# Kernel optimization log

Measured on AMD Instinct MI355X. Metric: run time of the kernel, lower is better.

Reference implementation:

```python
import jax, jax.numpy as jnp
import numpy as np

GH, GW = 1024, 1024  # image-like grid graph, N = GH*GW nodes


def _grid_edge_index(h, w):
    idx = np.arange(h * w, dtype=np.int32).reshape(h, w)
    r = np.concatenate([idx[:, :-1].ravel(), idx[:, 1:].ravel(), idx[:-1, :].ravel(), idx[1:, :].ravel()])
    c = np.concatenate([idx[:, 1:].ravel(), idx[:, :-1].ravel(), idx[1:, :].ravel(), idx[:-1, :].ravel()])
    return np.stack([r, c]).astype(np.int32)


def setup_inputs():
    key = jax.random.key(0)
    ks = jax.random.split(key, 10)
    n = GH * GW
    ei = jnp.asarray(_grid_edge_index(GH, GW))
    yy, xx = np.meshgrid(np.arange(GH), np.arange(GW), indexing="ij")
    pos = jnp.asarray((np.stack([xx, yy], -1).reshape(n, 2) / float(GH)).astype(np.float32))
    x = jax.random.normal(ks[0], (n, 5), jnp.float32)
    s1, s2, s3, s4 = 5 ** -0.5, 16 ** -0.5, 32 ** -0.5, 8 ** -0.5
    return {
        "x": x, "pos": pos, "edge_index": ei,
        "W1": jax.random.normal(ks[1], (5, 16), jnp.float32) * s1,
        "W1r": jax.random.normal(ks[2], (5, 16), jnp.float32) * s1,
        "b1": jnp.zeros((16,), jnp.float32),
        "W2": jax.random.normal(ks[3], (16, 32), jnp.float32) * s2,
        "W2r": jax.random.normal(ks[4], (16, 32), jnp.float32) * s2,
        "b2": jnp.zeros((32,), jnp.float32),
        "lin1_w": jax.random.normal(ks[5], (32, 8), jnp.float32) * s3,
        "lin1_b": jnp.zeros((8,), jnp.float32),
        "lin2_w": jax.random.normal(ks[6], (8, 2), jnp.float32) * s4,
        "lin2_b": jnp.zeros((2,), jnp.float32),
    }


def _spline_conv_k1(x, row, col, evalid, W, Wr, b, n):
    # SplineConv(dim=1, kernel_size=1): single basis fn == 1, edge_attr cancels.
    # out_i = mean_{(j->i)} x_j @ W + x_i @ Wr + b   (aggr='mean', target = col)
    xw = x @ W
    seg = jnp.where(evalid, col, n)  # invalid edges -> dump segment n
    msg = jnp.where(evalid[:, None], xw[row], 0.0)
    s = jax.ops.segment_sum(msg, seg, num_segments=n + 1)[:n]
    cnt = jax.ops.segment_sum(evalid.astype(x.dtype), seg, num_segments=n + 1)[:n]
    return s / jnp.maximum(cnt, 1.0)[:, None] + x @ Wr + b


def _normalized_cut(row, col, edge_attr, evalid, n):
    seg = jnp.where(evalid, row, n)
    deg = jax.ops.segment_sum(evalid.astype(edge_attr.dtype), seg, num_segments=n + 1)[:n]
    inv = jnp.where(deg > 0, 1.0 / jnp.maximum(deg, 1.0), 0.0)
    return edge_attr * (inv[row] + inv[col])


def _heavy_edge_match(row, col, w, evalid, n):
    # graclus-style heavy-edge matching, deterministic parallel mutual-max variant:
    # each node proposes its max-weight neighbor; mutual proposals merge.
    ar = jnp.arange(n, dtype=jnp.int32)
    seg = jnp.where(evalid, row, n)
    wm = jnp.where(evalid, w, -jnp.inf)
    best = jax.ops.segment_max(wm, seg, num_segments=n + 1)[:n]
    is_best = evalid & (w == best[row])
    partner = jax.ops.segment_min(jnp.where(is_best, col, n), seg, num_segments=n + 1)[:n]
    partner = jnp.where(partner >= n, ar, partner).astype(jnp.int32)
    mutual = partner[partner] == ar
    return jnp.where(mutual, jnp.minimum(ar, partner), ar)


def _forward(x, pos, edge_index, W1, W1r, b1, W2, W2r, b2, lin1_w, lin1_b, lin2_w, lin2_b):
    n = x.shape[0]
    row, col = edge_index[0], edge_index[1]
    ev0 = jnp.ones(row.shape[0], dtype=bool)
    ar = jnp.arange(n, dtype=jnp.int32)

    # GNN1: relu(SplineConv) then LeakyReLU(0.1)
    x1 = jax.nn.leaky_relu(jax.nn.relu(_spline_conv_k1(x, row, col, ev0, W1, W1r, b1, n)), 0.1)

    # normalized_cut_2d on 1-d pseudo-pos x0[:,0]; graclus; max_pool
    attr1 = jnp.abs(x[row, 0] - x[col, 0])
    c1 = _heavy_edge_match(row, col, _normalized_cut(row, col, attr1, ev0, n), ev0, n)
    valid1 = c1 == ar
    xp = jax.ops.segment_max(x1, c1, num_segments=n)  # cluster-wise max pool
    xp = jnp.where(valid1[:, None], xp, 0.0)
    cnt1 = jax.ops.segment_sum(jnp.ones((n,), x.dtype), c1, num_segments=n)
    posp = jax.ops.segment_sum(pos, c1, num_segments=n) / jnp.maximum(cnt1, 1.0)[:, None]
    row2, col2 = c1[row], c1[col]
    ev2 = row2 != col2  # drop intra-cluster (self-loop) edges

    # GNN2 (kernel_size=1 => pooled Cartesian edge_attr unused) + LeakyReLU(0.1)
    x2 = jax.nn.leaky_relu(jax.nn.relu(_spline_conv_k1(xp, row2, col2, ev2, W2, W2r, b2, n)), 0.1)

    # normalized_cut on pooled 2-d pos; graclus; max_pool_x; global_mean_pool
    d = posp[row2] - posp[col2]
    attr2 = jnp.sqrt(jnp.sum(d * d, axis=1) + 1e-12)
    c2 = _heavy_edge_match(row2, col2, _normalized_cut(row2, col2, attr2, ev2, n), ev2, n)
    seg2 = jnp.where(valid1, c2, n)
    x3 = jax.ops.segment_max(x2, seg2, num_segments=n + 1)[:n]
    cnt2 = jax.ops.segment_sum(valid1.astype(x.dtype), seg2, num_segments=n + 1)[:n]
    valid2 = cnt2 > 0
    x3 = jnp.where(valid2[:, None], x3, 0.0)
    pooled = jnp.sum(x3, axis=0) / jnp.sum(valid2.astype(x.dtype))  # single graph -> mean over clusters

    h = jax.nn.leaky_relu(pooled @ lin1_w + lin1_b, 0.1)
    return h @ lin2_w + lin2_b  # == x[0], shape [2]


def reference(x, pos, edge_index, W1, W1r, b1, W2, W2r, b2, lin1_w, lin1_b, lin2_w, lin2_b):
    return _forward(x, pos, edge_index, W1, W1r, b1, W2, W2r, b2, lin1_w, lin1_b, lin2_w, lin2_b)
```

## Files before the change

kernel.cpp:

```cpp
#include <hip/hip_runtime.h>
#include <math.h>

typedef long long i64;
typedef unsigned long long u64;

#define GWD 1024
#define GMSK 1023
#define GSH 10

__device__ __forceinline__ int deg_of(int m) {
  int xx = m & GMSK, yy = m >> GSH;
  return (xx > 0) + (xx < GMSK) + (yy > 0) + (yy < GMSK);
}

__global__ __launch_bounds__(256)
void kA_match1(const float* __restrict__ x, int* __restrict__ partner1, int n) {
#pragma clang fp contract(off)
  int m = blockIdx.x * 256 + threadIdx.x;
  if (m >= n) return;
  int xx = m & GMSK, yy = m >> GSH;
  bool vW = xx > 0, vE = xx < GMSK, vN = yy > 0, vS = yy < GMSK;
  int cnt = (int)vW + (int)vE + (int)vN + (int)vS;
  float invi = 1.0f / (float)cnt;
  float xm0 = x[(i64)m * 5];
  float best = -INFINITY;
  int pr = n;
#define NB1(valid, J)                                                  \
  if (valid) {                                                         \
    int j = (J);                                                       \
    float a0 = x[(i64)j * 5];                                          \
    float w = fabsf(xm0 - a0) * (invi + 1.0f / (float)deg_of(j));      \
    if (w > best) { best = w; pr = j; }                                \
  }
  NB1(vN, m - GWD)
  NB1(vW, m - 1)
  NB1(vE, m + 1)
  NB1(vS, m + GWD)
#undef NB1
  partner1[m] = pr;
}

__device__ __forceinline__ void conv1_static(const float* __restrict__ x, int m,
                                             const float* w1, const float* w1r,
                                             const float* b1, float (&out)[16]) {
  int xx = m & GMSK, yy = m >> GSH;
  bool vW = xx > 0, vE = xx < GMSK, vN = yy > 0, vS = yy < GMSK;
  int cnt = (int)vW + (int)vE + (int)vN + (int)vS;
  float s0 = 0.f, s1 = 0.f, s2 = 0.f, s3 = 0.f, s4 = 0.f;
#define ACC1(valid, J)                                     \
  if (valid) {                                             \
    const float* xj = x + (i64)(J) * 5;                    \
    s0 += xj[0]; s1 += xj[1]; s2 += xj[2];                 \
    s3 += xj[3]; s4 += xj[4];                              \
  }
  ACC1(vN, m - GWD)
  ACC1(vW, m - 1)
  ACC1(vE, m + 1)
  ACC1(vS, m + GWD)
#undef ACC1
  const float* xm = x + (i64)m * 5;
  float m0 = xm[0], m1 = xm[1], m2 = xm[2], m3 = xm[3], m4 = xm[4];
  float cf = (float)cnt;
#pragma unroll
  for (int f = 0; f < 16; ++f) {
    float a  = s0 * w1[f] + s1 * w1[16 + f] + s2 * w1[32 + f] + s3 * w1[48 + f] + s4 * w1[64 + f];
    float rt = m0 * w1r[f] + m1 * w1r[16 + f] + m2 * w1r[32 + f] + m3 * w1r[48 + f] + m4 * w1r[64 + f];
    out[f] = fmaxf(a / cf + rt + b1[f], 0.0f);
  }
}

__global__ __launch_bounds__(256)
void kB_pool1(const float* __restrict__ x, const float* __restrict__ pos,
              const int* __restrict__ partner1,
              const float* __restrict__ W1, const float* __restrict__ W1r,
              const float* __restrict__ b1,
              int* __restrict__ c1, float* __restrict__ xp,
              float* __restrict__ posp, int n) {
  __shared__ float w1s[80], w1rs[80], b1s[16];
  for (int t = threadIdx.x; t < 80; t += 256) { w1s[t] = W1[t]; w1rs[t] = W1r[t]; }
  if (threadIdx.x < 16) b1s[threadIdx.x] = b1[threadIdx.x];
  __syncthreads();
  int m = blockIdx.x * 256 + threadIdx.x;
  if (m >= n) return;
  int p = partner1[m];
  bool mut = (partner1[p] == m);
  int head = mut ? min(m, p) : m;
  c1[m] = head;
  if (head != m) return;

  float px = pos[(i64)m * 2], py = pos[(i64)m * 2 + 1];
  if (mut) {
    px = (px + pos[(i64)p * 2]) * 0.5f;
    py = (py + pos[(i64)p * 2 + 1]) * 0.5f;
  }
  posp[(i64)m * 2] = px;
  posp[(i64)m * 2 + 1] = py;

  float v[16];
  conv1_static(x, m, w1s, w1rs, b1s, v);
  if (mut) {
    float u[16];
    conv1_static(x, p, w1s, w1rs, b1s, u);
#pragma unroll
    for (int f = 0; f < 16; ++f) v[f] = fmaxf(v[f], u[f]);
  }
#pragma unroll
  for (int f = 0; f < 16; ++f) xp[(i64)m * 16 + f] = v[f];
}

__device__ __forceinline__ int dcount(const int* __restrict__ c1, int q, int cq) {
  int xx = q & GMSK, yy = q >> GSH;
  int d = 0;
  if (yy > 0    && c1[q - GWD] != cq) ++d;
  if (xx > 0    && c1[q - 1]   != cq) ++d;
  if (xx < GMSK && c1[q + 1]   != cq) ++d;
  if (yy < GMSK && c1[q + GWD] != cq) ++d;
  return d;
}

__global__ __launch_bounds__(256)
void kC_deg2(const int* __restrict__ partner1, const int* __restrict__ c1,
             int* __restrict__ deg2, int n) {
  int m = blockIdx.x * 256 + threadIdx.x;
  if (m >= n) return;
  if (c1[m] != m) return;
  int p = partner1[m];
  bool mut = (partner1[p] == m);
  int d = dcount(c1, m, m);
  if (mut) d += dcount(c1, p, m);
  deg2[m] = d;
}

__global__ __launch_bounds__(256)
void kD_match2(const int* __restrict__ partner1, const int* __restrict__ c1,
               const float* __restrict__ posp, const int* __restrict__ deg2,
               int* __restrict__ partner2, int n) {
#pragma clang fp contract(off)
  int i = blockIdx.x * 256 + threadIdx.x;
  if (i >= n) return;
  if (c1[i] != i) return;
  int p = partner1[i];
  bool mut = (partner1[p] == i);
  float pix = posp[(i64)i * 2], piy = posp[(i64)i * 2 + 1];
  int di = deg2[i];
  float invi = (di > 0) ? 1.0f / (float)di : 0.0f;
  float best = -INFINITY;
  int bc = n;
#define NB2(valid, J)                                                   \
  if (valid) {                                                          \
    int j = (J);                                                        \
    int cu = c1[j];                                                     \
    if (cu != i) {                                                      \
      float dx = pix - posp[(i64)cu * 2];                               \
      float dy = piy - posp[(i64)cu * 2 + 1];                           \
      float attr = sqrtf((dx * dx + dy * dy) + 1e-12f);                 \
      int dc = deg2[cu];                                                \
      float invc = (dc > 0) ? 1.0f / (float)dc : 0.0f;                  \
      float w = attr * (invi + invc);                                   \
      if (w > best) { best = w; bc = cu; }                              \
      else if (w == best && cu < bc) bc = cu;                           \
    }                                                                   \
  }
  {
    int xx = i & GMSK, yy = i >> GSH;
    NB2(yy > 0, i - GWD)
    NB2(xx > 0, i - 1)
    NB2(xx < GMSK, i + 1)
    NB2(yy < GMSK, i + GWD)
  }
  if (mut) {
    int qx = p & GMSK, qy = p >> GSH;
    NB2(qy > 0, p - GWD)
    NB2(qx > 0, p - 1)
    NB2(qx < GMSK, p + 1)
    NB2(qy < GMSK, p + GWD)
  }
#undef NB2
  partner2[i] = (bc >= n) ? i : bc;
}

__device__ __forceinline__ bool l2head(const int* __restrict__ c1,
                                       const int* __restrict__ partner2, int i, int n) {
  if (i >= n || c1[i] != i) return false;
  int p2 = partner2[i];
  bool mut2 = (p2 != i) && (partner2[p2] == i);
  return !(mut2 && p2 < i);
}

__global__ __launch_bounds__(256)
void kP_count(const int* __restrict__ c1, const int* __restrict__ partner2,
              int* __restrict__ blockCounts, int n) {
  int i = blockIdx.x * 256 + threadIdx.x;
  bool a = l2head(c1, partner2, i, n);
  u64 b = __ballot(a);
  __shared__ int wc4[4];
  int lane = threadIdx.x & 63, wv = threadIdx.x >> 6;
  if (lane == 0) wc4[wv] = __popcll(b);
  __syncthreads();
  if (threadIdx.x == 0) blockCounts[blockIdx.x] = wc4[0] + wc4[1] + wc4[2] + wc4[3];
}

__global__ __launch_bounds__(256)
void kP_scan(const int* __restrict__ blockCounts, int* __restrict__ blockOffsets,
             int* __restrict__ countBuf, int nblk,
             const float* __restrict__ W2, const float* __restrict__ W2r,
             float* __restrict__ W2T, float* __restrict__ W2rT) {
  int t = threadIdx.x;
  for (int e = t; e < 512; e += 256) {
    int k = e >> 5, f = e & 31;
    W2T[f * 16 + k]  = W2[e];
    W2rT[f * 16 + k] = W2r[e];
  }
  __shared__ int tsum[256];
  __shared__ int toff[256];
  int per = (nblk + 255) / 256;
  int base = t * per;
  int s = 0;
  for (int k = 0; k < per; ++k) { int q = base + k; if (q < nblk) s += blockCounts[q]; }
  tsum[t] = s;
  __syncthreads();
  if (t == 0) {
    int a = 0;
    for (int k = 0; k < 256; ++k) { toff[k] = a; a += tsum[k]; }
    *countBuf = a;
  }
  __syncthreads();
  int off = toff[t];
  for (int k = 0; k < per; ++k) {
    int q = base + k;
    if (q < nblk) { blockOffsets[q] = off; off += blockCounts[q]; }
  }
}

__global__ __launch_bounds__(256)
void kP_write(const int* __restrict__ c1, const int* __restrict__ partner2,
              const int* __restrict__ blockOffsets, int* __restrict__ L, int n) {
  int i = blockIdx.x * 256 + threadIdx.x;
  bool a = l2head(c1, partner2, i, n);
  u64 b = __ballot(a);
  int lane = threadIdx.x & 63, wv = threadIdx.x >> 6;
  __shared__ int woff[4];
  if (lane == 0) woff[wv] = __popcll(b);
  __syncthreads();
  int pre = 0;
  for (int k = 0; k < wv; ++k) pre += woff[k];
  int rank = __popcll(b & ((lane == 0) ? 0ull : ((1ull << lane) - 1ull)));
  if (a) L[blockOffsets[blockIdx.x] + pre + rank] = i;
}

#define DECL16(P) \
  float P##0=0.f,P##1=0.f,P##2=0.f,P##3=0.f,P##4=0.f,P##5=0.f,P##6=0.f,P##7=0.f, \
        P##8=0.f,P##9=0.f,P##10=0.f,P##11=0.f,P##12=0.f,P##13=0.f,P##14=0.f,P##15=0.f

#define LOAD16(P, ptr) do { const float* _q=(ptr); \
  P##0=_q[0]; P##1=_q[1]; P##2=_q[2]; P##3=_q[3]; P##4=_q[4]; P##5=_q[5]; P##6=_q[6]; P##7=_q[7]; \
  P##8=_q[8]; P##9=_q[9]; P##10=_q[10]; P##11=_q[11]; P##12=_q[12]; P##13=_q[13]; P##14=_q[14]; P##15=_q[15]; } while(0)

#define ADD16(P, ptr) do { const float* _q=(ptr); \
  P##0+=_q[0]; P##1+=_q[1]; P##2+=_q[2]; P##3+=_q[3]; P##4+=_q[4]; P##5+=_q[5]; P##6+=_q[6]; P##7+=_q[7]; \
  P##8+=_q[8]; P##9+=_q[9]; P##10+=_q[10]; P##11+=_q[11]; P##12+=_q[12]; P##13+=_q[13]; P##14+=_q[14]; P##15+=_q[15]; } while(0)

#define MUL16(P, v) do { float _v=(v); \
  P##0*=_v; P##1*=_v; P##2*=_v; P##3*=_v; P##4*=_v; P##5*=_v; P##6*=_v; P##7*=_v; \
  P##8*=_v; P##9*=_v; P##10*=_v; P##11*=_v; P##12*=_v; P##13*=_v; P##14*=_v; P##15*=_v; } while(0)

#define GATHER_MEMBER(P, CNT, m, cid) do {                                      \
  int _m = (m); int _mx = _m & GMSK, _my = _m >> GSH;                            \
  if (_my > 0)    { int _c = c1[_m - GWD]; if (_c != (cid)) { ++CNT; ADD16(P, xp + (i64)_c * 16); } } \
  if (_mx > 0)    { int _c = c1[_m - 1];   if (_c != (cid)) { ++CNT; ADD16(P, xp + (i64)_c * 16); } } \
  if (_mx < GMSK) { int _c = c1[_m + 1];   if (_c != (cid)) { ++CNT; ADD16(P, xp + (i64)_c * 16); } } \
  if (_my < GMSK) { int _c = c1[_m + GWD]; if (_c != (cid)) { ++CNT; ADD16(P, xp + (i64)_c * 16); } } \
} while(0)

__global__ __launch_bounds__(256)
void kE6_conv2_reduce(const int* __restrict__ partner1, const int* __restrict__ c1,
                      const int* __restrict__ partner2, const float* __restrict__ xp,
                      const float* __restrict__ W2T, const float* __restrict__ W2rT,
                      const float* __restrict__ b2,
                      const int* __restrict__ L, const int* __restrict__ countBuf,
                      float* __restrict__ partials) {
  int count = *countBuf;
  if ((i64)blockIdx.x * 128 >= (i64)count) {
    if (threadIdx.x < 33) partials[(i64)threadIdx.x * gridDim.x + blockIdx.x] = 0.f;
    return;
  }
  int gt = blockIdx.x * 256 + threadIdx.x;
  int pi = gt >> 1;
  int which = gt & 1;
  bool active = pi < count;
  bool doconv = false;
  DECL16(s); DECL16(hh); int cnt = 0;
  if (active) {
    int h = L[pi];
    int p2 = partner2[h];
    bool mut2 = (p2 != h) && (partner2[p2] == h);
    int myhead = which ? p2 : h;
    doconv = (which == 0) || mut2;
    if (doconv) {
      int pm = partner1[myhead];
      bool mm = (partner1[pm] == myhead);
      GATHER_MEMBER(s, cnt, myhead, myhead);
      if (mm) GATHER_MEMBER(s, cnt, pm, myhead);
      LOAD16(hh, xp + (i64)myhead * 16);
    }
  }
  float cf = (float)(cnt > 1 ? cnt : 1);
  float inv = 1.0f / cf;
  MUL16(s, inv);

  __shared__ float sm[4 * 33];
  int lane = threadIdx.x & 63, wv = threadIdx.x >> 6;

  for (int f = 0; f < 32; ++f) {
    const float4* wc = (const float4*)(W2T + (f << 4));
    float4 c0 = wc[0], c1v = wc[1], c2 = wc[2], c3 = wc[3];
    const float4* wr = (const float4*)(W2rT + (f << 4));
    float4 r0 = wr[0], r1 = wr[1], r2 = wr[2], r3 = wr[3];
    float bf = b2[f];
    float val = 0.f;
    if (doconv) {
      float a = s0 * c0.x + s1 * c0.y + s2 * c0.z + s3 * c0.w
              + s4 * c1v.x + s5 * c1v.y + s6 * c1v.z + s7 * c1v.w
              + s8 * c2.x + s9 * c2.y + s10 * c2.z + s11 * c2.w
              + s12 * c3.x + s13 * c3.y + s14 * c3.z + s15 * c3.w
              + hh0 * r0.x + hh1 * r0.y + hh2 * r0.z + hh3 * r0.w
              + hh4 * r1.x + hh5 * r1.y + hh6 * r1.z + hh7 * r1.w
              + hh8 * r2.x + hh9 * r2.y + hh10 * r2.z + hh11 * r2.w
              + hh12 * r3.x + hh13 * r3.y + hh14 * r3.z + hh15 * r3.w
              + bf;
      val = fmaxf(a, 0.0f);
    }
    float pmx = fmaxf(val, __shfl_xor(val, 1, 64));
    float contrib = (which == 0) ? pmx : 0.f;
    for (int o = 32; o >= 2; o >>= 1) contrib += __shfl_down(contrib, o, 64);
    if (lane == 0) sm[wv * 33 + f] = contrib;
  }
  {
    float v = (active && which == 0) ? 1.f : 0.f;
    for (int o = 32; o >= 2; o >>= 1) v += __shfl_down(v, o, 64);
    if (lane == 0) sm[wv * 33 + 32] = v;
  }
  __syncthreads();
  if (threadIdx.x < 33) {
    float v = sm[threadIdx.x] + sm[33 + threadIdx.x] + sm[66 + threadIdx.x] + sm[99 + threadIdx.x];
    partials[(i64)threadIdx.x * gridDim.x + blockIdx.x] = v;
  }
}

__global__ __launch_bounds__(256)
void kF1_rowsum(const float* __restrict__ partials, int NB, float* __restrict__ tot) {
  int r = blockIdx.x;
  const float* p = partials + (i64)r * NB;
  float a = 0.f;
  for (int k = threadIdx.x; k < NB; k += 256) a += p[k];
  __shared__ float sm[256];
  sm[threadIdx.x] = a;
  __syncthreads();
  for (int s = 128; s > 0; s >>= 1) {
    if (threadIdx.x < s) sm[threadIdx.x] += sm[threadIdx.x + s];
    __syncthreads();
  }
  if (threadIdx.x == 0) tot[r] = sm[0];
}

__global__ __launch_bounds__(64)
void kF2_mlp(const float* __restrict__ tot,
             const float* __restrict__ lin1w, const float* __restrict__ lin1b,
             const float* __restrict__ lin2w, const float* __restrict__ lin2b,
             float* __restrict__ out) {
  if (threadIdx.x != 0) return;
  float cnt = tot[32];
  float pooled[32];
#pragma unroll
  for (int f = 0; f < 32; ++f) pooled[f] = tot[f] / cnt;
  float h[8];
#pragma unroll
  for (int j = 0; j < 8; ++j) {
    float a = 0.f;
#pragma unroll
    for (int k = 0; k < 32; ++k) a += pooled[k] * lin1w[k * 8 + j];
    a += lin1b[j];
    h[j] = a >= 0.f ? a : 0.1f * a;
  }
#pragma unroll
  for (int m = 0; m < 2; ++m) {
    float a = 0.f;
#pragma unroll
    for (int j = 0; j < 8; ++j) a += h[j] * lin2w[j * 2 + m];
    out[m] = a + lin2b[m];
  }
}

extern "C" void kernel_launch(void* const* d_in, const int* in_sizes, int n_in,
                              void* d_out, int out_size, void* d_ws, size_t ws_size,
                              hipStream_t stream) {
  const float* x   = (const float*)d_in[0];
  const float* pos = (const float*)d_in[1];
  const float* W1  = (const float*)d_in[3];
  const float* W1r = (const float*)d_in[4];
  const float* b1  = (const float*)d_in[5];
  const float* W2  = (const float*)d_in[6];
  const float* W2r = (const float*)d_in[7];
  const float* b2  = (const float*)d_in[8];
  const float* l1w = (const float*)d_in[9];
  const float* l1b = (const float*)d_in[10];
  const float* l2w = (const float*)d_in[11];
  const float* l2b = (const float*)d_in[12];
  float* out = (float*)d_out;

  const int n = in_sizes[0] / 5;
  const int B = 256;
  const int gn = (n + B - 1) / B;
  const int ge = 2 * gn;

  float* base = (float*)d_ws;
  i64 off = 0;
  float* xp       = base + off; off += (i64)16 * n;
  float* posp     = base + off; off += (i64)2 * n;
  int*   partner1 = (int*)(base + off); off += n;
  int*   c1       = (int*)(base + off); off += n;
  int*   deg2     = (int*)(base + off); off += n;
  int*   partner2 = (int*)(base + off); off += n;
  int*   L        = (int*)(base + off); off += n;
  int*   blkCnt   = (int*)(base + off); off += gn;
  int*   blkOff   = (int*)(base + off); off += gn;
  int*   countBuf = (int*)(base + off); off += 1;
  off = (off + 3) & ~(i64)3;
  float* W2T      = base + off; off += 512;
  float* W2rT     = base + off; off += 512;
  float* partials = base + off; off += (i64)33 * ge;
  float* tot      = base + off; off += 33;
  (void)ws_size; (void)n_in; (void)out_size;

  kA_match1<<<gn, B, 0, stream>>>(x, partner1, n);
  kB_pool1<<<gn, B, 0, stream>>>(x, pos, partner1, W1, W1r, b1, c1, xp, posp, n);
  kC_deg2<<<gn, B, 0, stream>>>(partner1, c1, deg2, n);
  kD_match2<<<gn, B, 0, stream>>>(partner1, c1, posp, deg2, partner2, n);
  kP_count<<<gn, B, 0, stream>>>(c1, partner2, blkCnt, n);
  kP_scan<<<1, 256, 0, stream>>>(blkCnt, blkOff, countBuf, gn, W2, W2r, W2T, W2rT);
  kP_write<<<gn, B, 0, stream>>>(c1, partner2, blkOff, L, n);
  kE6_conv2_reduce<<<ge, B, 0, stream>>>(partner1, c1, partner2, xp, W2T, W2rT, b2,
                                         L, countBuf, partials);
  kF1_rowsum<<<33, 256, 0, stream>>>(partials, ge, tot);
  kF2_mlp<<<1, 64, 0, stream>>>(tot, l1w, l1b, l2w, l2b, out);
}
```

Measured before the change: 223.5 us.

## Use persistent fixed grid for conv2 reduce with per-thread accumulators

Replaces the one-item-per-thread conv2 reduction, which launched 2*gn blocks and ran 32 wave shuffle-reductions per block, with a fixed 1024-block grid. Each block loops over a contiguous chunk of the cluster list and keeps 32 feature accumulators in registers. One shared-memory reduction runs at the end, and a 0.5 factor corrects for both lanes of a pair adding the same max. This cuts per-item shuffle and reduction overhead and shrinks the partials array, at the cost of higher register pressure, a 36KB shared buffer that limits occupancy, and a serial 256-row sum per block.

```diff
diff --git a/kernel.cpp b/kernel.cpp
--- a/kernel.cpp
+++ b/kernel.cpp
@@ -7,6 +7,7 @@
 #define GWD 1024
 #define GMSK 1023
 #define GSH 10
+#define NBE 1024
 
 __device__ __forceinline__ int deg_of(int m) {
   int xx = m & GMSK, yy = m >> GSH;
@@ -272,30 +273,59 @@
   if (_my < GMSK) { int _c = c1[_m + GWD]; if (_c != (cid)) { ++CNT; ADD16(P, xp + (i64)_c * 16); } } \
 } while(0)
 
-__global__ __launch_bounds__(256)
-void kE6_conv2_reduce(const int* __restrict__ partner1, const int* __restrict__ c1,
+#define FSTEP(F) { \
+    const float4* wcp = (const float4*)(W2T + ((F) << 4)); \
+    float4 wa = wcp[0], wb = wcp[1], wcc = wcp[2], wd = wcp[3]; \
+    const float4* wrp = (const float4*)(W2rT + ((F) << 4)); \
+    float4 ra = wrp[0], rb = wrp[1], rc = wrp[2], rd = wrp[3]; \
+    float bfv = b2[(F)]; \
+    float val = 0.f; \
+    if (doconv) { \
+      float aa = s0*wa.x + s1*wa.y + s2*wa.z + s3*wa.w \
+               + s4*wb.x + s5*wb.y + s6*wb.z + s7*wb.w \
+               + s8*wcc.x + s9*wcc.y + s10*wcc.z + s11*wcc.w \
+               + s12*wd.x + s13*wd.y + s14*wd.z + s15*wd.w \
+               + hh0*ra.x + hh1*ra.y + hh2*ra.z + hh3*ra.w \
+               + hh4*rb.x + hh5*rb.y + hh6*rb.z + hh7*rb.w \
+               + hh8*rc.x + hh9*rc.y + hh10*rc.z + hh11*rc.w \
+               + hh12*rd.x + hh13*rd.y + hh14*rd.z + hh15*rd.w \
+               + bfv; \
+      val = fmaxf(aa, 0.0f); \
+    } \
+    float pmx = fmaxf(val, __shfl_xor(val, 1, 64)); \
+    q##F += pmx; }
+
+__global__ __launch_bounds__(256)
+void kE8_conv2_reduce(const int* __restrict__ partner1, const int* __restrict__ c1,
                       const int* __restrict__ partner2, const float* __restrict__ xp,
                       const float* __restrict__ W2T, const float* __restrict__ W2rT,
                       const float* __restrict__ b2,
                       const int* __restrict__ L, const int* __restrict__ countBuf,
                       float* __restrict__ partials) {
+  __shared__ float red[256][36];
   int count = *countBuf;
-  if ((i64)blockIdx.x * 128 >= (i64)count) {
-    if (threadIdx.x < 33) partials[(i64)threadIdx.x * gridDim.x + blockIdx.x] = 0.f;
-    return;
-  }
-  int gt = blockIdx.x * 256 + threadIdx.x;
-  int pi = gt >> 1;
-  int which = gt & 1;
-  bool active = pi < count;
-  bool doconv = false;
-  DECL16(s); DECL16(hh); int cnt = 0;
-  if (active) {
+  int b = blockIdx.x;
+  int w = (b & 7) * (NBE >> 3) + (b >> 3);
+  int chunk = (count + NBE - 1) / NBE;
+  int base = w * chunk;
+  int end = base + chunk; if (end > count) end = count;
+
+  int tid = threadIdx.x;
+  int which = tid & 1;
+
+  float q0=0.f,q1=0.f,q2=0.f,q3=0.f,q4=0.f,q5=0.f,q6=0.f,q7=0.f,
+        q8=0.f,q9=0.f,q10=0.f,q11=0.f,q12=0.f,q13=0.f,q14=0.f,q15=0.f,
+        q16=0.f,q17=0.f,q18=0.f,q19=0.f,q20=0.f,q21=0.f,q22=0.f,q23=0.f,
+        q24=0.f,q25=0.f,q26=0.f,q27=0.f,q28=0.f,q29=0.f,q30=0.f,q31=0.f;
+  float ccount = 0.f;
+
+  for (int pi = base + (tid >> 1); pi < end; pi += 128) {
     int h = L[pi];
     int p2 = partner2[h];
     bool mut2 = (p2 != h) && (partner2[p2] == h);
     int myhead = which ? p2 : h;
-    doconv = (which == 0) || mut2;
+    bool doconv = (which == 0) || mut2;
+    DECL16(s); DECL16(hh); int cnt = 0;
     if (doconv) {
       int pm = partner1[myhead];
       bool mm = (partner1[pm] == myhead);
@@ -303,47 +333,30 @@
       if (mm) GATHER_MEMBER(s, cnt, pm, myhead);
       LOAD16(hh, xp + (i64)myhead * 16);
     }
-  }
-  float cf = (float)(cnt > 1 ? cnt : 1);
-  float inv = 1.0f / cf;
-  MUL16(s, inv);
-
-  __shared__ float sm[4 * 33];
-  int lane = threadIdx.x & 63, wv = threadIdx.x >> 6;
-
-  for (int f = 0; f < 32; ++f) {
-    const float4* wc = (const float4*)(W2T + (f << 4));
-    float4 c0 = wc[0], c1v = wc[1], c2 = wc[2], c3 = wc[3];
-    const float4* wr = (const float4*)(W2rT + (f << 4));
-    float4 r0 = wr[0], r1 = wr[1], r2 = wr[2], r3 = wr[3];
-    float bf = b2[f];
-    float val = 0.f;
-    if (doconv) {
-      float a = s0 * c0.x + s1 * c0.y + s2 * c0.z + s3 * c0.w
-              + s4 * c1v.x + s5 * c1v.y + s6 * c1v.z + s7 * c1v.w
-              + s8 * c2.x + s9 * c2.y + s10 * c2.z + s11 * c2.w
-              + s12 * c3.x + s13 * c3.y + s14 * c3.z + s15 * c3.w
-              + hh0 * r0.x + hh1 * r0.y + hh2 * r0.z + hh3 * r0.w
-              + hh4 * r1.x + hh5 * r1.y + hh6 * r1.z + hh7 * r1.w
-              + hh8 * r2.x + hh9 * r2.y + hh10 * r2.z + hh11 * r2.w
-              + hh12 * r3.x + hh13 * r3.y + hh14 * r3.z + hh15 * r3.w
-              + bf;
-      val = fmaxf(a, 0.0f);
-    }
-    float pmx = fmaxf(val, __shfl_xor(val, 1, 64));
-    float contrib = (which == 0) ? pmx : 0.f;
-    for (int o = 32; o >= 2; o >>= 1) contrib += __shfl_down(contrib, o, 64);
-    if (lane == 0) sm[wv * 33 + f] = contrib;
-  }
-  {
-    float v = (active && which == 0) ? 1.f : 0.f;
-    for (int o = 32; o >= 2; o >>= 1) v += __shfl_down(v, o, 64);
-    if (lane == 0) sm[wv * 33 + 32] = v;
-  }
-  __syncthreads();
-  if (threadIdx.x < 33) {
-    float v = sm[threadIdx.x] + sm[33 + threadIdx.x] + sm[66 + threadIdx.x] + sm[99 + threadIdx.x];
-    partials[(i64)threadIdx.x * gridDim.x + blockIdx.x] = v;
+    float inv = 1.0f / (float)(cnt > 1 ? cnt : 1);
+    MUL16(s, inv);
+
+    FSTEP(0)  FSTEP(1)  FSTEP(2)  FSTEP(3)  FSTEP(4)  FSTEP(5)  FSTEP(6)  FSTEP(7)
+    FSTEP(8)  FSTEP(9)  FSTEP(10) FSTEP(11) FSTEP(12) FSTEP(13) FSTEP(14) FSTEP(15)
+    FSTEP(16) FSTEP(17) FSTEP(18) FSTEP(19) FSTEP(20) FSTEP(21) FSTEP(22) FSTEP(23)
+    FSTEP(24) FSTEP(25) FSTEP(26) FSTEP(27) FSTEP(28) FSTEP(29) FSTEP(30) FSTEP(31)
+    ccount += 1.f;
+  }
+
+  red[tid][0]=q0;  red[tid][1]=q1;  red[tid][2]=q2;  red[tid][3]=q3;
+  red[tid][4]=q4;  red[tid][5]=q5;  red[tid][6]=q6;  red[tid][7]=q7;
+  red[tid][8]=q8;  red[tid][9]=q9;  red[tid][10]=q10; red[tid][11]=q11;
+  red[tid][12]=q12; red[tid][13]=q13; red[tid][14]=q14; red[tid][15]=q15;
+  red[tid][16]=q16; red[tid][17]=q17; red[tid][18]=q18; red[tid][19]=q19;
+  red[tid][20]=q20; red[tid][21]=q21; red[tid][22]=q22; red[tid][23]=q23;
+  red[tid][24]=q24; red[tid][25]=q25; red[tid][26]=q26; red[tid][27]=q27;
+  red[tid][28]=q28; red[tid][29]=q29; red[tid][30]=q30; red[tid][31]=q31;
+  red[tid][32]=ccount;
+  __syncthreads();
+  if (tid < 33) {
+    float ssum = 0.f;
+    for (int rr = 0; rr < 256; ++rr) ssum += red[rr][tid];
+    partials[(i64)tid * NBE + b] = ssum * 0.5f;
   }
 }
 
@@ -411,7 +424,6 @@
   const int n = in_sizes[0] / 5;
   const int B = 256;
   const int gn = (n + B - 1) / B;
-  const int ge = 2 * gn;
 
   float* base = (float*)d_ws;
   i64 off = 0;
@@ -428,7 +440,7 @@
   off = (off + 3) & ~(i64)3;
   float* W2T      = base + off; off += 512;
   float* W2rT     = base + off; off += 512;
-  float* partials = base + off; off += (i64)33 * ge;
+  float* partials = base + off; off += (i64)33 * NBE;
   float* tot      = base + off; off += 33;
   (void)ws_size; (void)n_in; (void)out_size;
 
@@ -439,8 +451,8 @@
   kP_count<<<gn, B, 0, stream>>>(c1, partner2, blkCnt, n);
   kP_scan<<<1, 256, 0, stream>>>(blkCnt, blkOff, countBuf, gn, W2, W2r, W2T, W2rT);
   kP_write<<<gn, B, 0, stream>>>(c1, partner2, blkOff, L, n);
-  kE6_conv2_reduce<<<ge, B, 0, stream>>>(partner1, c1, partner2, xp, W2T, W2rT, b2,
-                                         L, countBuf, partials);
-  kF1_rowsum<<<33, 256, 0, stream>>>(partials, ge, tot);
+  kE8_conv2_reduce<<<NBE, B, 0, stream>>>(partner1, c1, partner2, xp, W2T, W2rT, b2,
+                                          L, countBuf, partials);
+  kF1_rowsum<<<33, 256, 0, stream>>>(partials, NBE, tot);
   kF2_mlp<<<1, 64, 0, stream>>>(tot, l1w, l1b, l2w, l2b, out);
 }
```

After: 256.8 us. 14.9% more time.
